# Kernel optimization log

Measured on AMD Instinct MI355X. Metric: run time of the kernel, lower is better.

The kernel has to match this reference:

```python
import jax, jax.numpy as jnp
import numpy as np

EPS = 1e-8


def cos_loss(a, b):
    # a, b: [n, c, h, w]; cosine distance over channel dim, mean over rest
    a_norm = jnp.sqrt((a * a).sum(1, keepdims=True))
    b_norm = jnp.sqrt((b * b).sum(1, keepdims=True))
    cossim = ((a / (a_norm + EPS)) * (b / (b_norm + EPS))).sum(1)
    return (1.0 - cossim).mean()


def nn_feat_replace(a, b):
    # a: [1, c, h, w], b: [1, c, h2, w2]
    n, c, h, w = a.shape
    a_flat = a.reshape(n, c, -1)                    # [1, c, hw]
    b_flat = b.reshape(n, c, -1)                    # [1, c, h2w2]
    # normalize along channel dim (matches argmin_cos_distance's two-eps scheme)
    b_n = b_flat / (jnp.sqrt((b_flat * b_flat).sum(1, keepdims=True) + EPS) + EPS)
    a_n = a_flat / (jnp.sqrt((a_flat * a_flat).sum(1, keepdims=True) + EPS) + EPS)
    # full cosine-distance matrix: [1, hw, h2w2]
    d_mat = 1.0 - jnp.einsum('bci,bcj->bij', a_n, b_n)
    z_best = jnp.argmin(d_mat, axis=2)              # [1, hw]
    feat = jnp.take(b_flat, z_best[0], axis=2)      # gather: [1, c, hw]
    return feat.reshape(n, c, h, w)


def setup_inputs() -> dict:
    key = jax.random.key(0)
    k1, k2 = jax.random.split(key)
    a = jax.random.normal(k1, (1, 768, 128, 128), dtype=jnp.float32)
    b = jax.random.normal(k2, (1, 768, 128, 128), dtype=jnp.float32)
    return {"a": a, "b": b}


def reference(a, b):
    target = nn_feat_replace(a, b)
    return cos_loss(a, target)
```

## Files before the change

### kernel.cpp

```cpp
#include <hip/hip_runtime.h>
#include <stdint.h>

#define HW 16384
#define CDIM 768
#define EPSF 1e-8f

typedef float f32x4  __attribute__((ext_vector_type(4)));
typedef float f32x16 __attribute__((ext_vector_type(16)));
typedef int   i32x8  __attribute__((ext_vector_type(8)));
typedef uint32_t u32x4 __attribute__((ext_vector_type(4)));

__device__ inline void async16(const void* g, void* l) {
    __builtin_amdgcn_global_load_lds(
        (const __attribute__((address_space(1))) uint32_t*)g,
        (__attribute__((address_space(3))) uint32_t*)l, 16, 0, 0);
}

__device__ inline uint32_t pk4_fp8(float v0, float v1, float v2, float v3) {
    uint32_t r = __builtin_amdgcn_cvt_pk_fp8_f32(v0, v1, 0, false);
    r = __builtin_amdgcn_cvt_pk_fp8_f32(v2, v3, r, true);
    return r;
}

__global__ void __launch_bounds__(256)
transpose_fp8_norm(const float* __restrict__ a, const float* __restrict__ b,
                   uint8_t* __restrict__ at8, uint8_t* __restrict__ bn8,
                   float* __restrict__ sumsq_a, float* __restrict__ sumsq_b) {
    const int z = blockIdx.z;
    const float* src = z ? b : a;
    uint8_t* dst = z ? bn8 : at8;
    float* sums = z ? sumsq_b : sumsq_a;
    const float mult = z ? 8.0f : 16.0f;

    __shared__ float tile[64][65];
    const int s0 = blockIdx.x * 64, c0 = blockIdx.y * 64;
    const int tx = threadIdx.x & 63, ty = threadIdx.x >> 6;
#pragma unroll
    for (int p = 0; p < 16; ++p) {
        int cl = p * 4 + ty;
        tile[cl][tx] = src[(size_t)(c0 + cl) * HW + s0 + tx];
    }
    __syncthreads();

    const int chgrp = tx & 15, rowsub = tx >> 4;
    uint32_t* dst32 = (uint32_t*)dst;
#pragma unroll
    for (int p = 0; p < 4; ++p) {
        int sl = p * 16 + ty * 4 + rowsub;
        float v0 = tile[chgrp * 4 + 0][sl];
        float v1 = tile[chgrp * 4 + 1][sl];
        float v2 = tile[chgrp * 4 + 2][sl];
        float v3 = tile[chgrp * 4 + 3][sl];
        float part = v0 * v0 + v1 * v1 + v2 * v2 + v3 * v3;
        dst32[(size_t)(s0 + sl) * (CDIM / 4) + (c0 >> 2) + chgrp] =
            pk4_fp8(v0 * mult, v1 * mult, v2 * mult, v3 * mult);
#pragma unroll
        for (int m = 1; m < 16; m <<= 1) part += __shfl_xor(part, m, 64);
        if (chgrp == 0) atomicAdd(&sums[s0 + sl], part);
    }
}

__global__ void
gemm_argmax(const uint8_t* __restrict__ at8, const uint8_t* __restrict__ bn8,
            const float* __restrict__ sumsq_b,
            unsigned long long* __restrict__ best) {
    __shared__ uint8_t Al[128 * 128];
    __shared__ uint8_t Bl[128 * 128];

    const int g = blockIdx.x;
    const int xcd    = g & 7;
    const int s      = g >> 3;
    const int super  = s >> 5;
    const int within = s & 31;
    const int si = super >> 4;
    const int sj = super & 15;
    const int it = xcd * 16 + si * 4 + (within & 3);
    const int jt = sj * 8 + (within >> 2);

    const int i0 = it * 128, j0 = jt * 128;
    const int tid = threadIdx.x;
    const int lane = tid & 63, w = tid >> 6;
    const int wi = w & 1, wj = w >> 1;
    const int l31 = lane & 31, hi = lane >> 5;

    f32x16 acc[2][2] = {};

    const int srow = lane >> 3;
    const int schunk = ((lane & 7) ^ srow) * 16;
    const uint8_t* gA = at8 + (size_t)(i0 + w * 32 + srow) * CDIM + schunk;
    const uint8_t* gB = bn8 + (size_t)(j0 + w * 32 + srow) * CDIM + schunk;
    uint8_t* lA = &Al[w * 32 * 128];
    uint8_t* lB = &Bl[w * 32 * 128];

    const int rA0 = (wi * 64 + l31) * 128;
    const int rB0 = (wj * 64 + l31) * 128;
    const int cks0 = (((0) + hi * 2) ^ (lane & 7)) * 16;
    const int cks1 = (((4) + hi * 2) ^ (lane & 7)) * 16;

#pragma unroll 1
    for (int kk = 0; kk < CDIM; kk += 128) {
#pragma unroll
        for (int e = 0; e < 4; ++e) {
            async16(gA + kk + e * 8 * CDIM, lA + e * 1024);
            async16(gB + kk + e * 8 * CDIM, lB + e * 1024);
        }
        __syncthreads();

#pragma unroll
        for (int ks = 0; ks < 2; ++ks) {
            const int c0 = ks ? cks1 : cks0;
            i32x8 af0, af1, bg;
            *(u32x4*)&af0       = *(const u32x4*)&Al[rA0 + c0];
            *((u32x4*)&af0 + 1) = *(const u32x4*)&Al[rA0 + (c0 ^ 16)];
            *(u32x4*)&af1       = *(const u32x4*)&Al[rA0 + 4096 + c0];
            *((u32x4*)&af1 + 1) = *(const u32x4*)&Al[rA0 + 4096 + (c0 ^ 16)];

            *(u32x4*)&bg        = *(const u32x4*)&Bl[rB0 + c0];
            *((u32x4*)&bg + 1)  = *(const u32x4*)&Bl[rB0 + (c0 ^ 16)];
            acc[0][0] = __builtin_amdgcn_mfma_scale_f32_32x32x64_f8f6f4(
                bg, af0, acc[0][0], 0, 0, 0, 0x7F7F7F7F, 0, 0x7F7F7F7F);
            acc[0][1] = __builtin_amdgcn_mfma_scale_f32_32x32x64_f8f6f4(
                bg, af1, acc[0][1], 0, 0, 0, 0x7F7F7F7F, 0, 0x7F7F7F7F);

            *(u32x4*)&bg        = *(const u32x4*)&Bl[rB0 + 4096 + c0];
            *((u32x4*)&bg + 1)  = *(const u32x4*)&Bl[rB0 + 4096 + (c0 ^ 16)];
            acc[1][0] = __builtin_amdgcn_mfma_scale_f32_32x32x64_f8f6f4(
                bg, af0, acc[1][0], 0, 0, 0, 0x7F7F7F7F, 0, 0x7F7F7F7F);
            acc[1][1] = __builtin_amdgcn_mfma_scale_f32_32x32x64_f8f6f4(
                bg, af1, acc[1][1], 0, 0, 0, 0x7F7F7F7F, 0, 0x7F7F7F7F);
        }
        __syncthreads();
    }

    float bv[2] = {-1e30f, -1e30f};
    int   bj[2] = {0, 0};
#pragma unroll
    for (int nj = 0; nj < 2; ++nj) {
        float invd[16];
#pragma unroll
        for (int r = 0; r < 16; ++r) {
            int j = j0 + wj * 64 + nj * 32 + (r & 3) + 8 * (r >> 2) + 4 * hi;
            invd[r] = 1.0f / (sqrtf(sumsq_b[j] + EPSF) + EPSF);
        }
#pragma unroll
        for (int mi = 0; mi < 2; ++mi) {
#pragma unroll
            for (int r = 0; r < 16; ++r) {
                int j = j0 + wj * 64 + nj * 32 + (r & 3) + 8 * (r >> 2) + 4 * hi;
                float v = acc[nj][mi][r] * invd[r];
                if (v > bv[mi] || (v == bv[mi] && j < bj[mi])) {
                    bv[mi] = v; bj[mi] = j;
                }
            }
        }
    }
#pragma unroll
    for (int mi = 0; mi < 2; ++mi) {
        float ov = __shfl_xor(bv[mi], 32, 64);
        int   oj = __shfl_xor(bj[mi], 32, 64);
        if (ov > bv[mi] || (ov == bv[mi] && oj < bj[mi])) {
            bv[mi] = ov; bj[mi] = oj;
        }
        if (hi == 0) {
            int gi = i0 + wi * 64 + mi * 32 + l31;
            uint32_t u = __float_as_uint(bv[mi]);
            u = (u & 0x80000000u) ? ~u : (u | 0x80000000u);
            unsigned long long packed =
                ((unsigned long long)u << 32) | (uint32_t)(~(uint32_t)bj[mi]);
            atomicMax(&best[gi], packed);
        }
    }
}

__global__ void loss_reduce(const unsigned long long* __restrict__ best,
                            const float* __restrict__ sumsq_a,
                            const float* __restrict__ sumsq_b,
                            float* __restrict__ out) {
    int i = blockIdx.x * 256 + threadIdx.x;
    unsigned long long pk = best[i];
    uint32_t x = (uint32_t)(pk >> 32);
    float v = (x & 0x80000000u) ? __uint_as_float(x & 0x7fffffffu)
                                : __uint_as_float(~x);
    int j = (int)(~(uint32_t)pk);
    float sb = sumsq_b[j];
    float denb = sqrtf(sb + EPSF) + EPSF;
    float dot = v * denb * (1.0f / 128.0f);
    float cs = dot / ((sqrtf(sumsq_a[i]) + EPSF) * (sqrtf(sb) + EPSF));
    float term = 1.0f - cs;
#pragma unroll
    for (int m = 32; m; m >>= 1) term += __shfl_down(term, m, 64);
    __shared__ float red[4];
    int wv = threadIdx.x >> 6, lane = threadIdx.x & 63;
    if (lane == 0) red[wv] = term;
    __syncthreads();
    if (threadIdx.x == 0) {
        float ssum = (red[0] + red[1] + red[2] + red[3]) * (1.0f / HW);
        atomicAdd(out, ssum);
    }
}

extern "C" void kernel_launch(void* const* d_in, const int* in_sizes, int n_in,
                              void* d_out, int out_size, void* d_ws, size_t ws_size,
                              hipStream_t stream) {
    const float* a = (const float*)d_in[0];
    const float* b = (const float*)d_in[1];
    char* ws = (char*)d_ws;

    const size_t T_BYTES = (size_t)HW * CDIM;
    uint8_t* at8 = (uint8_t*)ws;
    uint8_t* bn8 = (uint8_t*)(ws + T_BYTES);
    float* sumsq_a = (float*)(ws + 2 * T_BYTES);
    float* sumsq_b = (float*)(ws + 2 * T_BYTES + HW * sizeof(float));
    unsigned long long* best =
        (unsigned long long*)(ws + 2 * T_BYTES + 2 * HW * sizeof(float));

    hipMemsetAsync(sumsq_a, 0, 2 * HW * sizeof(float) + HW * sizeof(unsigned long long),
                   stream);
    hipMemsetAsync(d_out, 0, out_size * sizeof(float), stream);

    dim3 tg(HW / 64, CDIM / 64, 2);
    transpose_fp8_norm<<<tg, 256, 0, stream>>>(a, b, at8, bn8, sumsq_a, sumsq_b);
    gemm_argmax<<<(HW / 128) * (HW / 128), 256, 0, stream>>>(at8, bn8, sumsq_b, best);
    loss_reduce<<<HW / 256, 256, 0, stream>>>(best, sumsq_a, sumsq_b, (float*)d_out);
}
```

Before: 418.5 us.

## Double-buffer K loop in 64-wide stages and precompute inverse b norms

The GEMM main loop now uses two 8 KB LDS buffers per operand with K steps of 64. The next stage's async global-to-LDS loads are issued while the current stage's MFMAs run, and there is one barrier per step instead of two. The per-column inverse norm of b is computed once in a separate small kernel, so the epilogue loads it with vector loads instead of recomputing sqrt and reciprocal in every block. The cost is more loop iterations with a vmcnt(0) wait each, a new swizzle pattern, and an extra kernel launch.

```diff
diff --git a/kernel.cpp b/kernel.cpp
--- a/kernel.cpp
+++ b/kernel.cpp
@@ -60,12 +60,18 @@
     }
 }
 
+__global__ void prep_invd(const float* __restrict__ sumsq_b,
+                          float* __restrict__ invdb) {
+    int j = blockIdx.x * 256 + threadIdx.x;
+    invdb[j] = 1.0f / (sqrtf(sumsq_b[j] + EPSF) + EPSF);
+}
+
 __global__ void
 gemm_argmax(const uint8_t* __restrict__ at8, const uint8_t* __restrict__ bn8,
-            const float* __restrict__ sumsq_b,
+            const float* __restrict__ invdb,
             unsigned long long* __restrict__ best) {
-    __shared__ uint8_t Al[128 * 128];
-    __shared__ uint8_t Bl[128 * 128];
+    __shared__ uint8_t Al[2 * 8192];
+    __shared__ uint8_t Bl[2 * 8192];
 
     const int g = blockIdx.x;
     const int xcd    = g & 7;
@@ -85,69 +91,78 @@
 
     f32x16 acc[2][2] = {};
 
-    const int srow = lane >> 3;
-    const int schunk = ((lane & 7) ^ srow) * 16;
+    const int srow = lane >> 2;
+    const int schunk = ((lane & 3) ^ ((lane >> 3) & 3)) * 16;
     const uint8_t* gA = at8 + (size_t)(i0 + w * 32 + srow) * CDIM + schunk;
     const uint8_t* gB = bn8 + (size_t)(j0 + w * 32 + srow) * CDIM + schunk;
-    uint8_t* lA = &Al[w * 32 * 128];
-    uint8_t* lB = &Bl[w * 32 * 128];
-
-    const int rA0 = (wi * 64 + l31) * 128;
-    const int rB0 = (wj * 64 + l31) * 128;
-    const int cks0 = (((0) + hi * 2) ^ (lane & 7)) * 16;
-    const int cks1 = (((4) + hi * 2) ^ (lane & 7)) * 16;
+    uint8_t* lA = Al + w * 2048;
+    uint8_t* lB = Bl + w * 2048;
+
+    const int rA0 = (wi * 64 + l31) * 64;
+    const int rB0 = (wj * 64 + l31) * 64;
+    const int c0 = ((hi * 2) ^ ((l31 >> 1) & 3)) * 16;
+
+#define STAGE(bo, kk)                                         \
+    do {                                                      \
+        async16(gA + (kk),             lA + (bo));            \
+        async16(gA + (kk) + 16 * CDIM, lA + (bo) + 1024);     \
+        async16(gB + (kk),             lB + (bo));            \
+        async16(gB + (kk) + 16 * CDIM, lB + (bo) + 1024);     \
+    } while (0)
+
+#define COMPUTE(bo)                                                          \
+    do {                                                                     \
+        i32x8 af0, af1, bg;                                                  \
+        *(u32x4*)&af0       = *(const u32x4*)&Al[(bo) + rA0 + c0];           \
+        *((u32x4*)&af0 + 1) = *(const u32x4*)&Al[(bo) + rA0 + (c0 ^ 16)];    \
+        *(u32x4*)&af1       = *(const u32x4*)&Al[(bo) + rA0 + 2048 + c0];    \
+        *((u32x4*)&af1 + 1) = *(const u32x4*)&Al[(bo) + rA0 + 2048 + (c0 ^ 16)]; \
+        *(u32x4*)&bg        = *(const u32x4*)&Bl[(bo) + rB0 + c0];           \
+        *((u32x4*)&bg + 1)  = *(const u32x4*)&Bl[(bo) + rB0 + (c0 ^ 16)];    \
+        acc[0][0] = __builtin_amdgcn_mfma_scale_f32_32x32x64_f8f6f4(         \
+            bg, af0, acc[0][0], 0, 0, 0, 0x7F7F7F7F, 0, 0x7F7F7F7F);         \
+        acc[0][1] = __builtin_amdgcn_mfma_scale_f32_32x32x64_f8f6f4(         \
+            bg, af1, acc[0][1], 0, 0, 0, 0x7F7F7F7F, 0, 0x7F7F7F7F);         \
+        *(u32x4*)&bg        = *(const u32x4*)&Bl[(bo) + rB0 + 2048 + c0];    \
+        *((u32x4*)&bg + 1)  = *(const u32x4*)&Bl[(bo) + rB0 + 2048 + (c0 ^ 16)]; \
+        acc[1][0] = __builtin_amdgcn_mfma_scale_f32_32x32x64_f8f6f4(         \
+            bg, af0, acc[1][0], 0, 0, 0, 0x7F7F7F7F, 0, 0x7F7F7F7F);         \
+        acc[1][1] = __builtin_amdgcn_mfma_scale_f32_32x32x64_f8f6f4(         \
+            bg, af1, acc[1][1], 0, 0, 0, 0x7F7F7F7F, 0, 0x7F7F7F7F);         \
+    } while (0)
+
+    STAGE(0, 0);
+    asm volatile("s_waitcnt vmcnt(0)" ::: "memory");
+    __builtin_amdgcn_s_barrier();
 
 #pragma unroll 1
-    for (int kk = 0; kk < CDIM; kk += 128) {
-#pragma unroll
-        for (int e = 0; e < 4; ++e) {
-            async16(gA + kk + e * 8 * CDIM, lA + e * 1024);
-            async16(gB + kk + e * 8 * CDIM, lB + e * 1024);
-        }
-        __syncthreads();
-
-#pragma unroll
-        for (int ks = 0; ks < 2; ++ks) {
-            const int c0 = ks ? cks1 : cks0;
-            i32x8 af0, af1, bg;
-            *(u32x4*)&af0       = *(const u32x4*)&Al[rA0 + c0];
-            *((u32x4*)&af0 + 1) = *(const u32x4*)&Al[rA0 + (c0 ^ 16)];
-            *(u32x4*)&af1       = *(const u32x4*)&Al[rA0 + 4096 + c0];
-            *((u32x4*)&af1 + 1) = *(const u32x4*)&Al[rA0 + 4096 + (c0 ^ 16)];
-
-            *(u32x4*)&bg        = *(const u32x4*)&Bl[rB0 + c0];
-            *((u32x4*)&bg + 1)  = *(const u32x4*)&Bl[rB0 + (c0 ^ 16)];
-            acc[0][0] = __builtin_amdgcn_mfma_scale_f32_32x32x64_f8f6f4(
-                bg, af0, acc[0][0], 0, 0, 0, 0x7F7F7F7F, 0, 0x7F7F7F7F);
-            acc[0][1] = __builtin_amdgcn_mfma_scale_f32_32x32x64_f8f6f4(
-                bg, af1, acc[0][1], 0, 0, 0, 0x7F7F7F7F, 0, 0x7F7F7F7F);
-
-            *(u32x4*)&bg        = *(const u32x4*)&Bl[rB0 + 4096 + c0];
-            *((u32x4*)&bg + 1)  = *(const u32x4*)&Bl[rB0 + 4096 + (c0 ^ 16)];
-            acc[1][0] = __builtin_amdgcn_mfma_scale_f32_32x32x64_f8f6f4(
-                bg, af0, acc[1][0], 0, 0, 0, 0x7F7F7F7F, 0, 0x7F7F7F7F);
-            acc[1][1] = __builtin_amdgcn_mfma_scale_f32_32x32x64_f8f6f4(
-                bg, af1, acc[1][1], 0, 0, 0, 0x7F7F7F7F, 0, 0x7F7F7F7F);
-        }
-        __syncthreads();
-    }
+    for (int t = 0; t < 11; ++t) {
+        const int bo = (t & 1) * 8192;
+        STAGE(bo ^ 8192, (t + 1) * 64);
+        COMPUTE(bo);
+        asm volatile("s_waitcnt vmcnt(0)" ::: "memory");
+        __builtin_amdgcn_s_barrier();
+    }
+    COMPUTE(8192);
+
+#undef STAGE
+#undef COMPUTE
 
     float bv[2] = {-1e30f, -1e30f};
     int   bj[2] = {0, 0};
 #pragma unroll
     for (int nj = 0; nj < 2; ++nj) {
-        float invd[16];
-#pragma unroll
-        for (int r = 0; r < 16; ++r) {
-            int j = j0 + wj * 64 + nj * 32 + (r & 3) + 8 * (r >> 2) + 4 * hi;
-            invd[r] = 1.0f / (sqrtf(sumsq_b[j] + EPSF) + EPSF);
-        }
+        const int jb = j0 + wj * 64 + nj * 32 + 4 * hi;
+        f32x4 iv[4];
+#pragma unroll
+        for (int q = 0; q < 4; ++q)
+            iv[q] = *(const f32x4*)&invdb[jb + 8 * q];
 #pragma unroll
         for (int mi = 0; mi < 2; ++mi) {
 #pragma unroll
             for (int r = 0; r < 16; ++r) {
-                int j = j0 + wj * 64 + nj * 32 + (r & 3) + 8 * (r >> 2) + 4 * hi;
-                float v = acc[nj][mi][r] * invd[r];
+                int j = jb + (r & 3) + 8 * (r >> 2);
+                float v = acc[nj][mi][r] * iv[r >> 2][r & 3];
                 if (v > bv[mi] || (v == bv[mi] && j < bj[mi])) {
                     bv[mi] = v; bj[mi] = j;
                 }
@@ -213,6 +228,8 @@
     float* sumsq_b = (float*)(ws + 2 * T_BYTES + HW * sizeof(float));
     unsigned long long* best =
         (unsigned long long*)(ws + 2 * T_BYTES + 2 * HW * sizeof(float));
+    float* invdb = (float*)(ws + 2 * T_BYTES + 2 * HW * sizeof(float)
+                            + HW * sizeof(unsigned long long));
 
     hipMemsetAsync(sumsq_a, 0, 2 * HW * sizeof(float) + HW * sizeof(unsigned long long),
                    stream);
@@ -220,6 +237,7 @@
 
     dim3 tg(HW / 64, CDIM / 64, 2);
     transpose_fp8_norm<<<tg, 256, 0, stream>>>(a, b, at8, bn8, sumsq_a, sumsq_b);
-    gemm_argmax<<<(HW / 128) * (HW / 128), 256, 0, stream>>>(at8, bn8, sumsq_b, best);
+    prep_invd<<<HW / 256, 256, 0, stream>>>(sumsq_b, invdb);
+    gemm_argmax<<<(HW / 128) * (HW / 128), 256, 0, stream>>>(at8, bn8, invdb, best);
     loss_reduce<<<HW / 256, 256, 0, stream>>>(best, sumsq_a, sumsq_b, (float*)d_out);
 }
```

Measured after the change: 376.0 us. -10.2%, faster.
